# Kernel optimization log

Hardware: AMD Instinct MI355X
Metric: run time of the kernel (lower is better)

The kernel has to match this reference:

```python
import jax, jax.numpy as jnp
import numpy as np

N_NODES = 20000
N_EDGES = 320000
HIDDEN = 512
EDGE_DIM = 64
LN_EPS = 1e-5


def mish(x):
    return x * jnp.tanh(jax.nn.softplus(x))


def setup_inputs() -> dict:
    key = jax.random.key(0)
    ks = jax.random.split(key, 8)
    s = lambda fan_in: 1.0 / np.sqrt(fan_in)
    return {
        "x": jax.random.normal(ks[0], (N_NODES, HIDDEN), dtype=jnp.float32),
        "edge_index": jax.random.randint(ks[1], (2, N_EDGES), 0, N_NODES, dtype=jnp.int64),
        "edge_attr": jax.random.normal(ks[2], (N_EDGES, EDGE_DIM), dtype=jnp.float32),
        "W1": jax.random.normal(ks[3], (2 * HIDDEN + EDGE_DIM, HIDDEN), dtype=jnp.float32) * s(2 * HIDDEN + EDGE_DIM),
        "b1": jnp.zeros((HIDDEN,), dtype=jnp.float32),
        "W2": jax.random.normal(ks[4], (HIDDEN, HIDDEN), dtype=jnp.float32) * s(HIDDEN),
        "b2": jnp.zeros((HIDDEN,), dtype=jnp.float32),
        "W3": jax.random.normal(ks[5], (2 * HIDDEN, HIDDEN), dtype=jnp.float32) * s(2 * HIDDEN),
        "b3": jnp.zeros((HIDDEN,), dtype=jnp.float32),
        "W4": jax.random.normal(ks[6], (HIDDEN, HIDDEN), dtype=jnp.float32) * s(HIDDEN),
        "b4": jnp.zeros((HIDDEN,), dtype=jnp.float32),
        "gamma": jnp.ones((HIDDEN,), dtype=jnp.float32),
        "beta": jnp.zeros((HIDDEN,), dtype=jnp.float32),
    }


def reference(x, edge_index, edge_attr, W1, b1, W2, b2, W3, b3, W4, b4, gamma, beta):
    src, dst = edge_index[0], edge_index[1]
    # msg_mlp: Linear -> Mish -> Linear -> Mish on [E, 2H+Edim]
    edge_feat = jnp.concatenate([x[src], x[dst], edge_attr], axis=-1)  # [E, 2H+Edim]
    h = mish(edge_feat @ W1 + b1)
    messages = mish(h @ W2 + b2)  # [E, H]
    # scatter-add messages to destination nodes
    agg = jax.ops.segment_sum(messages, dst, num_segments=x.shape[0])  # [N, H]
    # update_mlp: Linear -> Mish -> Linear
    u = mish(jnp.concatenate([x, agg], axis=-1) @ W3 + b3)
    out = u @ W4 + b4  # [N, H]
    # residual + LayerNorm
    y = x + out
    mu = jnp.mean(y, axis=-1, keepdims=True)
    var = jnp.mean(jnp.square(y - mu), axis=-1, keepdims=True)
    return (y - mu) * jax.lax.rsqrt(var + LN_EPS) * gamma + beta
```

## Files before the change

### kernel.cpp

```cpp
#include <hip/hip_runtime.h>
#include <cstdint>
#include <cstddef>

#define NNODES 20000
#define NEDGES 320000
#define HID 512
#define EDIM 64
#define KFEAT (2*HID + EDIM)

typedef __bf16 bf16x8 __attribute__((ext_vector_type(8)));
typedef short short8 __attribute__((ext_vector_type(8)));
typedef float f32x4 __attribute__((ext_vector_type(4)));

#define AM_NODE 1
#define AM_DIR  2
#define EP_BF16    0
#define EP_F32     2
#define EP_BF16L   3
#define EP_RAW     5

__device__ __forceinline__ uint16_t f2bf(float f){
  uint32_t u = __float_as_uint(f);
  u += 0x7FFFu + ((u >> 16) & 1u);
  return (uint16_t)(u >> 16);
}
__device__ __forceinline__ float bf2f(uint16_t h){
  return __uint_as_float((uint32_t)h << 16);
}
__device__ __forceinline__ float mishf(float v){
  float e = __expf(fminf(v, 18.f));
  float n = e * (e + 2.f);
  return v * __fdividef(n, n + 2.f);
}
__device__ __forceinline__ void gl_lds16(const void* g, void* l){
  __builtin_amdgcn_global_load_lds(
      (const __attribute__((address_space(1))) uint32_t*)g,
      (__attribute__((address_space(3))) uint32_t*)l, 16, 0, 0);
}

__global__ void detect_idx(const int* __restrict__ e, int* __restrict__ flag){
  int i = blockIdx.x * 256 + threadIdx.x;
  if (e[2*i + 1] != 0) atomicOr(flag, 1);
}
__global__ void norm_idx(const int* __restrict__ e, const int* __restrict__ flag,
                         int* __restrict__ s, int* __restrict__ d){
  int i = blockIdx.x * 256 + threadIdx.x;
  if (i >= NEDGES) return;
  int sv, dv;
  if (*flag){ sv = e[i];     dv = e[NEDGES + i]; }
  else      { sv = e[2*i];   dv = e[2*NEDGES + 2*i]; }
  sv = sv < 0 ? 0 : (sv > NNODES-1 ? NNODES-1 : sv);
  dv = dv < 0 ? 0 : (dv > NNODES-1 ? NNODES-1 : dv);
  s[i] = sv; d[i] = dv;
}

__global__ void hist_k(const int* __restrict__ d, int* __restrict__ cnt){
  int i = blockIdx.x * 256 + threadIdx.x;
  if (i < NEDGES) atomicAdd(&cnt[d[i]], 1);
}
__global__ __launch_bounds__(256)
void scan_k(const int* __restrict__ cnt, int* __restrict__ rp, int* __restrict__ cur){
  const int SEG = (NNODES + 255) / 256;
  const int t = threadIdx.x;
  const int lo = t * SEG;
  const int hi = (lo + SEG < NNODES) ? lo + SEG : NNODES;
  int s = 0;
  for (int i = lo; i < hi; ++i) s += cnt[i];
  __shared__ int sh[256];
  sh[t] = s; __syncthreads();
  for (int o = 1; o < 256; o <<= 1){
    int v = (t >= o) ? sh[t - o] : 0;
    __syncthreads();
    sh[t] += v;
    __syncthreads();
  }
  int pre = t ? sh[t-1] : 0;
  for (int i = lo; i < hi; ++i){
    rp[i] = pre; cur[i] = pre; pre += cnt[i];
  }
  if (t == 255) rp[NNODES] = sh[255];
}
__global__ void permute_k(const int* __restrict__ srcN, const int* __restrict__ dstN,
                          int* __restrict__ cur, int* __restrict__ srcS,
                          int* __restrict__ eidx){
  int i = blockIdx.x * 256 + threadIdx.x;
  if (i < NEDGES){
    int d = dstN[i];
    int p = atomicAdd(&cur[d], 1);
    srcS[p] = srcN[i];
    eidx[p] = i;
  }
}
__global__ void fill_dstS(const int* __restrict__ rp, int* __restrict__ dstS){
  int n = blockIdx.x;
  int lo = rp[n], hi = rp[n+1];
  for (int e = lo + threadIdx.x; e < hi; e += 64) dstS[e] = n;
}

__global__ void cast_bf16_vec(const float4* __restrict__ in, ushort4* __restrict__ out, int n4){
  int i = blockIdx.x * 256 + threadIdx.x;
  if (i < n4){
    float4 v = in[i];
    ushort4 o; o.x = f2bf(v.x); o.y = f2bf(v.y); o.z = f2bf(v.z); o.w = f2bf(v.w);
    out[i] = o;
  }
}
__global__ void transpose_cast(const float* __restrict__ W, uint16_t* __restrict__ WT, int K, int N){
  int k = blockIdx.x * 256 + threadIdx.x;
  int n = blockIdx.y;
  if (k < K) WT[(size_t)n * K + k] = f2bf(W[(size_t)k * N + n]);
}

template<int AMODE, int EPI, int KTOT, int BPQ>
__global__ __launch_bounds__(256, 2)
void gemm_k(const uint16_t* __restrict__ A0, const uint16_t* __restrict__ A1,
            const uint16_t* __restrict__ BT, const float* __restrict__ bias,
            uint16_t* __restrict__ Cb, float* __restrict__ Cf,
            int bstr, int cstr, int m0base, int M, int crowOff)
{
  __shared__ __align__(16) char smem[32768];
  char* As = smem;
  char* Bs = smem + 16384;
  const int t = threadIdx.x;
  const int ntx = gridDim.x, nty = gridDim.y;
  int bx = blockIdx.x, by = blockIdx.y;
  if ((nty & 7) == 0){
    int flat = by * ntx + bx;
    int xcd = flat & 7;
    int i = flat >> 3;
    by = xcd * (nty >> 3) + i / ntx;
    bx = i % ntx;
  }
  const int m0 = m0base + by * 128;
  const int n0 = bx * 128;
  const int srow = t >> 3;
  const int c8   = t & 7;
  const int scol = ((c8 ^ (srow & 7)) << 3);
  const int ldst = srow * 128 + c8 * 16;

  const uint16_t* as0[4]; const uint16_t* as1[4];
  #pragma unroll
  for (int i = 0; i < 4; ++i){
    int gm = m0 + srow + 32*i;
    if (gm > M - 1) gm = M - 1;
    if (AMODE == AM_NODE){
      as0[i] = A0 + (size_t)gm * HID;
      as1[i] = A1 + (size_t)gm * HID;
    } else {
      as0[i] = A0 + (size_t)gm * KTOT;
      as1[i] = A0;
    }
  }
  const uint16_t* brow[4];
  #pragma unroll
  for (int i = 0; i < 4; ++i){
    int nr = n0 + srow + 32*i;
    if (BPQ) brow[i] = BT + (size_t)(nr & (HID-1))*bstr + (nr >> 9)*HID;
    else     brow[i] = BT + (size_t)nr*bstr;
  }

  const int lane = t & 63;
  const int wv = t >> 6;
  const int wm = (wv >> 1) * 64;
  const int wn = (wv & 1) * 64;
  const int l15 = lane & 15;
  const int lk16 = (lane >> 4) << 4;
  const int swz = (l15 & 7) << 4;

  f32x4 acc[4][4] = {};

  const int NK = KTOT / 64;
  for (int kk = 0; kk < NK; ++kk){
    const int k0 = kk * 64;
    #pragma unroll
    for (int i = 0; i < 4; ++i){
      const uint16_t* g;
      if (AMODE == AM_NODE){
        g = (k0 < HID) ? as0[i] + (k0 + scol) : as1[i] + (k0 - HID + scol);
      } else {
        g = as0[i] + (k0 + scol);
      }
      gl_lds16(g, As + i*4096 + ldst);
    }
    #pragma unroll
    for (int i = 0; i < 4; ++i)
      gl_lds16(brow[i] + (k0 + scol), Bs + i*4096 + ldst);
    __syncthreads();
    #pragma unroll
    for (int ks = 0; ks < 2; ++ks){
      bf16x8 af[4], bfr[4];
      #pragma unroll
      for (int i = 0; i < 4; ++i){
        const int ar = wm + i*16 + l15;
        af[i] = *(const bf16x8*)(As + ar*128 + ((ks*64 + lk16) ^ swz));
      }
      #pragma unroll
      for (int j = 0; j < 4; ++j){
        const int br = wn + j*16 + l15;
        bfr[j] = *(const bf16x8*)(Bs + br*128 + ((ks*64 + lk16) ^ swz));
      }
      #pragma unroll
      for (int i = 0; i < 4; ++i)
        #pragma unroll
        for (int j = 0; j < 4; ++j)
          acc[i][j] = __builtin_amdgcn_mfma_f32_16x16x32_bf16(af[i], bfr[j], acc[i][j], 0, 0, 0);
    }
    __syncthreads();
  }

  #pragma unroll
  for (int i = 0; i < 4; ++i){
    const int rb = wm + i*16 + ((lane >> 4) << 2);
    #pragma unroll
    for (int j = 0; j < 4; ++j){
      const int gcol = n0 + wn + j*16 + l15;
      const float bv = (EPI == EP_BF16L || EPI == EP_RAW) ? 0.f : bias[gcol];
      #pragma unroll
      for (int r = 0; r < 4; ++r){
        const int grow = m0 + rb + r;
        if (grow < M){
          float v = acc[i][j][r] + bv;
          if (EPI == EP_BF16){
            Cb[(size_t)(grow - crowOff) * cstr + gcol] = f2bf(mishf(v));
          } else if (EPI == EP_BF16L || EPI == EP_RAW){
            Cb[(size_t)(grow - crowOff) * cstr + gcol] = f2bf(v);
          } else {
            Cf[(size_t)grow * cstr + gcol] = v;
          }
        }
      }
    }
  }
}

__global__ __launch_bounds__(256, 4)
void eh_k(const uint16_t* __restrict__ eab, const uint16_t* __restrict__ PQb,
          const int* __restrict__ idx,
          const uint16_t* __restrict__ w1t, const float* __restrict__ b1,
          uint16_t* __restrict__ hb, int m0base, int crowOff)
{
  __shared__ __align__(16) char smem[32768];
  const int t = threadIdx.x;
  const int m0 = m0base + blockIdx.x * 32;
  const int lane = t & 63;
  const int wv = t >> 6;
  const int l15 = lane & 15;
  const int lg = lane >> 4;
  const int* srcS = idx;
  const int* dstS = idx + NEDGES;
  const int* eidx = idx + 2*NEDGES;

  int eidxr[2];
  #pragma unroll
  for (int fr = 0; fr < 2; ++fr) eidxr[fr] = eidx[m0 + fr*16 + l15];

  f32x4 acc[2][8] = {};

  #pragma unroll
  for (int ks = 0; ks < 2; ++ks){
    bf16x8 bF[8];
    #pragma unroll
    for (int fc = 0; fc < 8; ++fc){
      int n = wv*128 + fc*16 + l15;
      bF[fc] = *(const bf16x8*)(w1t + (size_t)n*KFEAT + 2*HID + ks*32 + lg*8);
    }
    #pragma unroll
    for (int fr = 0; fr < 2; ++fr){
      bf16x8 av = *(const bf16x8*)(eab + (size_t)eidxr[fr]*EDIM + ks*32 + lg*8);
      #pragma unroll
      for (int fc = 0; fc < 8; ++fc)
        acc[fr][fc] = __builtin_amdgcn_mfma_f32_16x16x32_bf16(av, bF[fc], acc[fr][fc], 0, 0, 0);
    }
  }

  char* slab = smem + wv*8192;
  const float4 b1v0 = *(const float4*)(b1 + wv*128 + l15*4);
  const float4 b1v1 = *(const float4*)(b1 + wv*128 + 64 + l15*4);
  #pragma unroll
  for (int fr = 0; fr < 2; ++fr){
    #pragma unroll
    for (int fc = 0; fc < 8; ++fc){
      #pragma unroll
      for (int r = 0; r < 4; ++r){
        int row = lg*4 + r;
        int cb = ((fc*16 + l15)*4) ^ ((lg & 1) << 6);
        *(float*)(slab + row*512 + cb) = acc[fr][fc][r];
      }
    }
    asm volatile("s_waitcnt lgkmcnt(0)" ::: "memory");
    __builtin_amdgcn_sched_barrier(0);
    #pragma unroll
    for (int i = 0; i < 4; ++i){
      int row = i*4 + lg;
      int grow = m0 + fr*16 + row;
      int s = srcS[grow];
      int d = dstS[grow];
      float4 v0 = *(const float4*)(slab + row*512 + ((l15*16) ^ ((i & 1) << 6)));
      float4 v1 = *(const float4*)(slab + row*512 + ((256 + l15*16) ^ ((i & 1) << 6)));
      ushort4 p0 = *(const ushort4*)(PQb + (size_t)s*1024 + wv*128 + l15*4);
      ushort4 p1 = *(const ushort4*)(PQb + (size_t)s*1024 + wv*128 + 64 + l15*4);
      ushort4 q0 = *(const ushort4*)(PQb + (size_t)d*1024 + 512 + wv*128 + l15*4);
      ushort4 q1 = *(const ushort4*)(PQb + (size_t)d*1024 + 512 + wv*128 + 64 + l15*4);
      ushort4 h0, h1;
      h0.x = f2bf(mishf(v0.x + bf2f(p0.x) + bf2f(q0.x) + b1v0.x));
      h0.y = f2bf(mishf(v0.y + bf2f(p0.y) + bf2f(q0.y) + b1v0.y));
      h0.z = f2bf(mishf(v0.z + bf2f(p0.z) + bf2f(q0.z) + b1v0.z));
      h0.w = f2bf(mishf(v0.w + bf2f(p0.w) + bf2f(q0.w) + b1v0.w));
      h1.x = f2bf(mishf(v1.x + bf2f(p1.x) + bf2f(q1.x) + b1v1.x));
      h1.y = f2bf(mishf(v1.y + bf2f(p1.y) + bf2f(q1.y) + b1v1.y));
      h1.z = f2bf(mishf(v1.z + bf2f(p1.z) + bf2f(q1.z) + b1v1.z));
      h1.w = f2bf(mishf(v1.w + bf2f(p1.w) + bf2f(q1.w) + b1v1.w));
      size_t hrow = (size_t)(grow - crowOff) * HID + wv*128;
      *(ushort4*)(hb + hrow + l15*4) = h0;
      *(ushort4*)(hb + hrow + 64 + l15*4) = h1;
    }
    asm volatile("s_waitcnt lgkmcnt(0)" ::: "memory");
    __builtin_amdgcn_sched_barrier(0);
  }
}

__global__ __launch_bounds__(128)
void gather_agg(const uint16_t* __restrict__ msg, const int* __restrict__ rp,
                const float* __restrict__ b2, float* __restrict__ agg,
                int e0, int e1){
  const int n = blockIdx.x;
  int lo = rp[n], hi = rp[n+1];
  if (lo < e0) lo = e0;
  if (hi > e1) hi = e1;
  if (lo >= hi) return;
  const int t = threadIdx.x;
  const float4 bv = ((const float4*)b2)[t];
  float4 a = {0.f, 0.f, 0.f, 0.f};
  for (int e = lo; e < hi; ++e){
    ushort4 m = ((const ushort4*)(msg + (size_t)(e - e0) * HID))[t];
    a.x += mishf(bf2f(m.x) + bv.x);
    a.y += mishf(bf2f(m.y) + bv.y);
    a.z += mishf(bf2f(m.z) + bv.z);
    a.w += mishf(bf2f(m.w) + bv.w);
  }
  float4* ap = ((float4*)(agg + (size_t)n * HID)) + t;
  float4 c = *ap;
  c.x += a.x; c.y += a.y; c.z += a.z; c.w += a.w;
  *ap = c;
}

__global__ __launch_bounds__(128)
void resid_ln(const float* __restrict__ x, const float* __restrict__ ob,
              const float* __restrict__ gamma, const float* __restrict__ beta,
              float* __restrict__ y){
  const int row = blockIdx.x;
  const int t = threadIdx.x;
  const float4 xv = ((const float4*)(x + (size_t)row * HID))[t];
  const float4 ov = ((const float4*)(ob + (size_t)row * HID))[t];
  float4 s4;
  s4.x = xv.x + ov.x; s4.y = xv.y + ov.y; s4.z = xv.z + ov.z; s4.w = xv.w + ov.w;
  float s = s4.x + s4.y + s4.z + s4.w;
  float q = s4.x*s4.x + s4.y*s4.y + s4.z*s4.z + s4.w*s4.w;
  #pragma unroll
  for (int o = 32; o; o >>= 1){
    s += __shfl_xor(s, o, 64);
    q += __shfl_xor(q, o, 64);
  }
  __shared__ float ss[2], qq[2];
  if ((t & 63) == 0){ ss[t >> 6] = s; qq[t >> 6] = q; }
  __syncthreads();
  const float S = ss[0] + ss[1], Q = qq[0] + qq[1];
  const float mu = S * (1.0f / HID);
  const float var = Q * (1.0f / HID) - mu * mu;
  const float inv = rsqrtf(var + 1e-5f);
  const float4 g = ((const float4*)gamma)[t];
  const float4 b = ((const float4*)beta)[t];
  float4 o;
  o.x = (s4.x - mu) * inv * g.x + b.x;
  o.y = (s4.y - mu) * inv * g.y + b.y;
  o.z = (s4.z - mu) * inv * g.z + b.z;
  o.w = (s4.w - mu) * inv * g.w + b.w;
  ((float4*)(y + (size_t)row * HID))[t] = o;
}

extern "C" void kernel_launch(void* const* d_in, const int* in_sizes, int n_in,
                              void* d_out, int out_size, void* d_ws, size_t ws_size,
                              hipStream_t stream)
{
  const float* x    = (const float*)d_in[0];
  const int*   ei   = (const int*)d_in[1];
  const float* ea   = (const float*)d_in[2];
  const float* W1   = (const float*)d_in[3];
  const float* b1   = (const float*)d_in[4];
  const float* W2   = (const float*)d_in[5];
  const float* b2   = (const float*)d_in[6];
  const float* W3   = (const float*)d_in[7];
  const float* b3   = (const float*)d_in[8];
  const float* W4   = (const float*)d_in[9];
  const float* b4   = (const float*)d_in[10];
  const float* gmm  = (const float*)d_in[11];
  const float* bet  = (const float*)d_in[12];
  float* out = (float*)d_out;

  uint8_t* w = (uint8_t*)d_ws;
  size_t off = 0;
  auto alloc = [&](size_t bytes) -> void* {
    void* p = w + off;
    off += (bytes + 255) & ~(size_t)255;
    return p;
  };
  uint16_t* xb   = (uint16_t*)alloc((size_t)NNODES*HID*2);
  uint16_t* w1t  = (uint16_t*)alloc((size_t)HID*KFEAT*2);
  uint16_t* w2t  = (uint16_t*)alloc((size_t)HID*HID*2);
  uint16_t* w3t  = (uint16_t*)alloc((size_t)HID*1024*2);
  uint16_t* w4t  = (uint16_t*)alloc((size_t)HID*HID*2);
  uint16_t* PQb  = (uint16_t*)alloc((size_t)NNODES*1024*2);
  float*    agg  = (float*)alloc((size_t)NNODES*HID*4);
  uint16_t* aggb = (uint16_t*)alloc((size_t)NNODES*HID*2);
  uint16_t* ub   = (uint16_t*)alloc((size_t)NNODES*HID*2);
  float*    outf = (float*)alloc((size_t)NNODES*HID*4);
  int*      srcN = (int*)alloc((size_t)NEDGES*4);
  int*      dstN = (int*)alloc((size_t)NEDGES*4);
  int*      idxS = (int*)alloc((size_t)NEDGES*4*3);
  int*      cnt  = (int*)alloc((size_t)NNODES*4);
  int*      rp   = (int*)alloc((size_t)(NNODES+1)*4);
  int*      cur  = (int*)alloc((size_t)NNODES*4);
  int*      flag = (int*)alloc(256);
  int*      srcS = idxS;
  int*      dstS = idxS + NEDGES;
  int*      eidx = idxS + 2*NEDGES;

  uint16_t* eab = (uint16_t*)outf;

  size_t remain = (ws_size > off) ? ws_size - off : 0;
  size_t maxChunk = remain / ((size_t)HID*2*2);
  long long chunkE = (long long)(maxChunk & ~(size_t)1023);
  if (chunkE > NEDGES) chunkE = NEDGES;
  if (chunkE < 1024) chunkE = 1024;
  uint16_t* hb   = (uint16_t*)alloc((size_t)chunkE*HID*2);
  uint16_t* msgb = (uint16_t*)alloc((size_t)chunkE*HID*2);

  hipMemsetAsync(agg, 0, (size_t)NNODES*HID*4, stream);
  hipMemsetAsync(cnt, 0, (size_t)NNODES*4, stream);
  hipMemsetAsync(flag, 0, 4, stream);

  detect_idx<<<64, 256, 0, stream>>>(ei, flag);
  norm_idx<<<(NEDGES+255)/256, 256, 0, stream>>>(ei, flag, srcN, dstN);
  hist_k<<<(NEDGES+255)/256, 256, 0, stream>>>(dstN, cnt);
  scan_k<<<1, 256, 0, stream>>>(cnt, rp, cur);
  permute_k<<<(NEDGES+255)/256, 256, 0, stream>>>(srcN, dstN, cur, srcS, eidx);
  fill_dstS<<<NNODES, 64, 0, stream>>>(rp, dstS);

  cast_bf16_vec<<<(NNODES*HID/4+255)/256, 256, 0, stream>>>((const float4*)x, (ushort4*)xb, NNODES*HID/4);
  cast_bf16_vec<<<(NEDGES*EDIM/4+255)/256, 256, 0, stream>>>((const float4*)ea, (ushort4*)eab, NEDGES*EDIM/4);

  transpose_cast<<<dim3((KFEAT+255)/256, HID), 256, 0, stream>>>(W1, w1t, KFEAT, HID);
  transpose_cast<<<dim3((HID+255)/256,   HID), 256, 0, stream>>>(W2, w2t, HID, HID);
  transpose_cast<<<dim3((1024+255)/256,  HID), 256, 0, stream>>>(W3, w3t, 1024, HID);
  transpose_cast<<<dim3((HID+255)/256,   HID), 256, 0, stream>>>(W4, w4t, HID, HID);

  dim3 gpq(1024/128, 160);
  gemm_k<AM_DIR, EP_BF16L, HID, 1><<<gpq, 256, 0, stream>>>(
      xb, nullptr, w1t, b1, PQb, nullptr, KFEAT, 1024, 0, NNODES, 0);

  for (long long e0 = 0; e0 < NEDGES; e0 += chunkE){
    int ce = (int)((NEDGES - e0 < chunkE) ? (NEDGES - e0) : chunkE);
    eh_k<<<(ce+31)/32, 256, 0, stream>>>(eab, PQb, idxS, w1t, b1, hb, (int)e0, (int)e0);
    dim3 g2(HID/128, (ce+127)/128);
    gemm_k<AM_DIR, EP_RAW, HID, 0><<<g2, 256, 0, stream>>>(
        hb, nullptr, w2t, b2, msgb, nullptr, HID, HID, 0, ce, 0);
    gather_agg<<<NNODES, 128, 0, stream>>>(msgb, rp, b2, agg, (int)e0, (int)(e0+ce));
  }

  cast_bf16_vec<<<(NNODES*HID/4+255)/256, 256, 0, stream>>>((const float4*)agg, (ushort4*)aggb, NNODES*HID/4);

  dim3 g3(HID/128, 160);
  gemm_k<AM_NODE, EP_BF16, 1024, 0><<<g3, 256, 0, stream>>>(
      xb, aggb, w3t, b3, ub, nullptr, 1024, HID, 0, NNODES, 0);
  gemm_k<AM_DIR, EP_F32, HID, 0><<<g3, 256, 0, stream>>>(
      ub, nullptr, w4t, b4, nullptr, outf, HID, HID, 0, NNODES, 0);

  resid_ln<<<NNODES, 128, 0, stream>>>(x, outf, gmm, bet, out);
}
```

Before: 912.9 us.

## Prefetch PQ rows in edge-hidden kernel and fuse agg bf16 cast into gather

The edge-hidden kernel now software-prefetches the next row's src/dst P/Q vectors from global memory while computing the current row, hiding gather latency behind the Mish epilogue. The final chunk's gather_agg also writes the bf16 copy of the aggregate, which removes the separate cast kernel and a full read of the fp32 aggregate. The aggb and ub buffers now alias the PQb region, which is dead after the edge loop, so workspace shrinks and larger edge chunks may fit. In exchange the prefetch adds register pressure, and the aliasing is only safe as long as PQb is not read after the last chunk.

```diff
diff --git a/kernel.cpp b/kernel.cpp
--- a/kernel.cpp
+++ b/kernel.cpp
@@ -254,8 +254,18 @@
   #pragma unroll
   for (int fr = 0; fr < 2; ++fr) eidxr[fr] = eidx[m0 + fr*16 + l15];
 
+  const int pqoff = wv*128 + l15*4;
+  ushort4 cp0, cp1, cq0, cq1, np0, np1, nq0, nq1;
+  {
+    int s0 = srcS[m0 + lg];
+    int d0 = dstS[m0 + lg];
+    const uint16_t* pb = PQb + (size_t)s0*1024 + pqoff;
+    const uint16_t* qb = PQb + (size_t)d0*1024 + 512 + pqoff;
+    cp0 = *(const ushort4*)pb;  cp1 = *(const ushort4*)(pb + 64);
+    cq0 = *(const ushort4*)qb;  cq1 = *(const ushort4*)(qb + 64);
+  }
+
   f32x4 acc[2][8] = {};
-
   #pragma unroll
   for (int ks = 0; ks < 2; ++ks){
     bf16x8 bF[8];
@@ -291,28 +301,34 @@
     __builtin_amdgcn_sched_barrier(0);
     #pragma unroll
     for (int i = 0; i < 4; ++i){
+      const int it = fr*4 + i;
+      if (it < 7){
+        int i2 = (it + 1) & 3, f2 = (it + 1) >> 2;
+        int row2 = i2*4 + lg;
+        int s = srcS[m0 + f2*16 + row2];
+        int d = dstS[m0 + f2*16 + row2];
+        const uint16_t* pb = PQb + (size_t)s*1024 + pqoff;
+        const uint16_t* qb = PQb + (size_t)d*1024 + 512 + pqoff;
+        np0 = *(const ushort4*)pb;  np1 = *(const ushort4*)(pb + 64);
+        nq0 = *(const ushort4*)qb;  nq1 = *(const ushort4*)(qb + 64);
+      }
       int row = i*4 + lg;
       int grow = m0 + fr*16 + row;
-      int s = srcS[grow];
-      int d = dstS[grow];
       float4 v0 = *(const float4*)(slab + row*512 + ((l15*16) ^ ((i & 1) << 6)));
       float4 v1 = *(const float4*)(slab + row*512 + ((256 + l15*16) ^ ((i & 1) << 6)));
-      ushort4 p0 = *(const ushort4*)(PQb + (size_t)s*1024 + wv*128 + l15*4);
-      ushort4 p1 = *(const ushort4*)(PQb + (size_t)s*1024 + wv*128 + 64 + l15*4);
-      ushort4 q0 = *(const ushort4*)(PQb + (size_t)d*1024 + 512 + wv*128 + l15*4);
-      ushort4 q1 = *(const ushort4*)(PQb + (size_t)d*1024 + 512 + wv*128 + 64 + l15*4);
       ushort4 h0, h1;
-      h0.x = f2bf(mishf(v0.x + bf2f(p0.x) + bf2f(q0.x) + b1v0.x));
-      h0.y = f2bf(mishf(v0.y + bf2f(p0.y) + bf2f(q0.y) + b1v0.y));
-      h0.z = f2bf(mishf(v0.z + bf2f(p0.z) + bf2f(q0.z) + b1v0.z));
-      h0.w = f2bf(mishf(v0.w + bf2f(p0.w) + bf2f(q0.w) + b1v0.w));
-      h1.x = f2bf(mishf(v1.x + bf2f(p1.x) + bf2f(q1.x) + b1v1.x));
-      h1.y = f2bf(mishf(v1.y + bf2f(p1.y) + bf2f(q1.y) + b1v1.y));
-      h1.z = f2bf(mishf(v1.z + bf2f(p1.z) + bf2f(q1.z) + b1v1.z));
-      h1.w = f2bf(mishf(v1.w + bf2f(p1.w) + bf2f(q1.w) + b1v1.w));
+      h0.x = f2bf(mishf(v0.x + bf2f(cp0.x) + bf2f(cq0.x) + b1v0.x));
+      h0.y = f2bf(mishf(v0.y + bf2f(cp0.y) + bf2f(cq0.y) + b1v0.y));
+      h0.z = f2bf(mishf(v0.z + bf2f(cp0.z) + bf2f(cq0.z) + b1v0.z));
+      h0.w = f2bf(mishf(v0.w + bf2f(cp0.w) + bf2f(cq0.w) + b1v0.w));
+      h1.x = f2bf(mishf(v1.x + bf2f(cp1.x) + bf2f(cq1.x) + b1v1.x));
+      h1.y = f2bf(mishf(v1.y + bf2f(cp1.y) + bf2f(cq1.y) + b1v1.y));
+      h1.z = f2bf(mishf(v1.z + bf2f(cp1.z) + bf2f(cq1.z) + b1v1.z));
+      h1.w = f2bf(mishf(v1.w + bf2f(cp1.w) + bf2f(cq1.w) + b1v1.w));
       size_t hrow = (size_t)(grow - crowOff) * HID + wv*128;
       *(ushort4*)(hb + hrow + l15*4) = h0;
       *(ushort4*)(hb + hrow + 64 + l15*4) = h1;
+      cp0 = np0; cp1 = np1; cq0 = nq0; cq1 = nq1;
     }
     asm volatile("s_waitcnt lgkmcnt(0)" ::: "memory");
     __builtin_amdgcn_sched_barrier(0);
@@ -322,12 +338,12 @@
 __global__ __launch_bounds__(128)
 void gather_agg(const uint16_t* __restrict__ msg, const int* __restrict__ rp,
                 const float* __restrict__ b2, float* __restrict__ agg,
-                int e0, int e1){
+                uint16_t* __restrict__ aggb, int e0, int e1, int fin){
   const int n = blockIdx.x;
   int lo = rp[n], hi = rp[n+1];
   if (lo < e0) lo = e0;
   if (hi > e1) hi = e1;
-  if (lo >= hi) return;
+  if (!fin && lo >= hi) return;
   const int t = threadIdx.x;
   const float4 bv = ((const float4*)b2)[t];
   float4 a = {0.f, 0.f, 0.f, 0.f};
@@ -341,7 +357,12 @@
   float4* ap = ((float4*)(agg + (size_t)n * HID)) + t;
   float4 c = *ap;
   c.x += a.x; c.y += a.y; c.z += a.z; c.w += a.w;
-  *ap = c;
+  if (lo < hi) *ap = c;
+  if (fin){
+    ushort4 o;
+    o.x = f2bf(c.x); o.y = f2bf(c.y); o.z = f2bf(c.z); o.w = f2bf(c.w);
+    ((ushort4*)(aggb + (size_t)n * HID))[t] = o;
+  }
 }
 
 __global__ __launch_bounds__(128)
@@ -411,8 +432,6 @@
   uint16_t* w4t  = (uint16_t*)alloc((size_t)HID*HID*2);
   uint16_t* PQb  = (uint16_t*)alloc((size_t)NNODES*1024*2);
   float*    agg  = (float*)alloc((size_t)NNODES*HID*4);
-  uint16_t* aggb = (uint16_t*)alloc((size_t)NNODES*HID*2);
-  uint16_t* ub   = (uint16_t*)alloc((size_t)NNODES*HID*2);
   float*    outf = (float*)alloc((size_t)NNODES*HID*4);
   int*      srcN = (int*)alloc((size_t)NEDGES*4);
   int*      dstN = (int*)alloc((size_t)NEDGES*4);
@@ -425,7 +444,9 @@
   int*      dstS = idxS + NEDGES;
   int*      eidx = idxS + 2*NEDGES;
 
-  uint16_t* eab = (uint16_t*)outf;
+  uint16_t* eab  = (uint16_t*)outf;
+  uint16_t* aggb = PQb;
+  uint16_t* ub   = PQb + (size_t)NNODES*HID;
 
   size_t remain = (ws_size > off) ? ws_size - off : 0;
   size_t maxChunk = remain / ((size_t)HID*2*2);
@@ -460,14 +481,14 @@
 
   for (long long e0 = 0; e0 < NEDGES; e0 += chunkE){
     int ce = (int)((NEDGES - e0 < chunkE) ? (NEDGES - e0) : chunkE);
+    int fin = (e0 + chunkE >= NEDGES) ? 1 : 0;
     eh_k<<<(ce+31)/32, 256, 0, stream>>>(eab, PQb, idxS, w1t, b1, hb, (int)e0, (int)e0);
     dim3 g2(HID/128, (ce+127)/128);
     gemm_k<AM_DIR, EP_RAW, HID, 0><<<g2, 256, 0, stream>>>(
         hb, nullptr, w2t, b2, msgb, nullptr, HID, HID, 0, ce, 0);
-    gather_agg<<<NNODES, 128, 0, stream>>>(msgb, rp, b2, agg, (int)e0, (int)(e0+ce));
-  }
-
-  cast_bf16_vec<<<(NNODES*HID/4+255)/256, 256, 0, stream>>>((const float4*)agg, (ushort4*)aggb, NNODES*HID/4);
+    gather_agg<<<NNODES, 128, 0, stream>>>(msgb, rp, b2, agg, aggb,
+                                           (int)e0, (int)(e0+ce), fin);
+  }
 
   dim3 g3(HID/128, 160);
   gemm_k<AM_NODE, EP_BF16, 1024, 0><<<g3, 256, 0, stream>>>(
```

Measured after the change: 915.1 us. About the same (+0.2%).
